# Performance work log

Hardware: AMD Instinct MI355X
Metric: run time of the kernel (lower is better)

Reference implementation:

```python
import jax, jax.numpy as jnp
import numpy as np
import math

B, S, D, H, DH = 1, 2048, 2048, 16, 64  # batch, seq, d_model, n_heads, d_head
LAMBDA_INIT = 0.8
EPS = 1e-5


def setup_inputs() -> dict:
    key = jax.random.key(0)
    ks = jax.random.split(key, 10)
    w_scale = 0.02
    inner = 2 * DH * H  # == D here
    return {
        "x": jax.random.normal(ks[0], (B, S, D), dtype=jnp.float32),
        "Wq": jax.random.normal(ks[1], (D, inner), dtype=jnp.float32) * w_scale,
        "Wk": jax.random.normal(ks[2], (D, inner), dtype=jnp.float32) * w_scale,
        "Wv": jax.random.normal(ks[3], (D, inner), dtype=jnp.float32) * w_scale,
        "Wo": jax.random.normal(ks[4], (inner, D), dtype=jnp.float32) * w_scale,
        "lambda_q1": jax.random.normal(ks[5], (DH,), dtype=jnp.float32) * 0.1,
        "lambda_k1": jax.random.normal(ks[6], (DH,), dtype=jnp.float32) * 0.1,
        "lambda_q2": jax.random.normal(ks[7], (DH,), dtype=jnp.float32) * 0.1,
        "lambda_k2": jax.random.normal(ks[8], (DH,), dtype=jnp.float32) * 0.1,
        "gn_weight": jnp.ones((inner,), dtype=jnp.float32),
        "gn_bias": jnp.zeros((inner,), dtype=jnp.float32),
    }


def reference(x, Wq, Wk, Wv, Wo, lambda_q1, lambda_k1, lambda_q2, lambda_k2,
              gn_weight, gn_bias):
    b, s, _ = x.shape
    dh = lambda_q1.shape[0]
    h = Wq.shape[1] // (2 * dh)
    scale = 1.0 / math.sqrt(dh)

    q = (x @ Wq).reshape(b, s, h, 2, dh)
    k = (x @ Wk).reshape(b, s, h, 2, dh)
    v = (x @ Wv).reshape(b, s, h, 2 * dh)

    # [B,H,S,dh]
    q1 = jnp.swapaxes(q[..., 0, :], 1, 2)
    q2 = jnp.swapaxes(q[..., 1, :], 1, 2)
    k1 = jnp.swapaxes(k[..., 0, :], 1, 2)
    k2 = jnp.swapaxes(k[..., 1, :], 1, 2)
    vh = jnp.swapaxes(v, 1, 2)  # [B,H,S,2*dh]

    score1 = jnp.einsum("bhsd,bhtd->bhst", q1, k1) * scale
    score2 = jnp.einsum("bhsd,bhtd->bhst", q2, k2) * scale
    attn1 = jax.nn.softmax(score1, axis=-1)
    attn2 = jax.nn.softmax(score2, axis=-1)

    lam = (jnp.exp(jnp.sum(lambda_q1 * lambda_k1))
           - jnp.exp(jnp.sum(lambda_q2 * lambda_k2)) + LAMBDA_INIT)

    out = jnp.einsum("bhst,bhtd->bhsd", attn1 - lam * attn2, vh)  # [B,H,S,2dh]
    out = jnp.swapaxes(out, 1, 2)  # [B,S,H,2dh]

    # GroupNorm: n_heads groups over the channel dim, per token
    mu = jnp.mean(out, axis=-1, keepdims=True)
    var = jnp.var(out, axis=-1, keepdims=True)
    out = (out - mu) * jax.lax.rsqrt(var + EPS)
    gw = gn_weight.reshape(h, 2 * dh)
    gb = gn_bias.reshape(h, 2 * dh)
    out = out * gw + gb

    out = out * (1.0 - LAMBDA_INIT)
    return out.reshape(b, s, -1) @ Wo
```

## Files before the change

kernel.cpp:

```cpp
#include <hip/hip_runtime.h>
#include <hip/hip_bf16.h>

typedef unsigned short u16;
typedef __attribute__((ext_vector_type(8))) short short8;
typedef __attribute__((ext_vector_type(4))) short short4v;
typedef __attribute__((ext_vector_type(4))) float f32x4;

#define S_DIM 2048
#define D_DIM 2048
#define H_NUM 16
#define DH_NUM 64

#if __has_builtin(__builtin_amdgcn_exp2f)
#define EXP2(x) __builtin_amdgcn_exp2f(x)
#else
#define EXP2(x) exp2f(x)
#endif

__device__ __forceinline__ u16 f2bf(float f) {
    union { float f; unsigned u; } x; x.f = f;
    unsigned r = x.u + 0x7fff + ((x.u >> 16) & 1);
    return (u16)(r >> 16);
}

__device__ __forceinline__ unsigned pk_bf16(float a, float b) {
    union { __hip_bfloat162 h; unsigned u; } cv;
    float2 t; t.x = a; t.y = b;
    cv.h = __float22bfloat162_rn(t);
    return cv.u;
}

__device__ __forceinline__ void lane_swap32(unsigned &a, unsigned &b) {
    asm("v_permlane32_swap_b32 %0, %1" : "+v"(a), "+v"(b));
}
__device__ __forceinline__ void lane_swap16(unsigned &a, unsigned &b) {
    asm("v_permlane16_swap_b32 %0, %1" : "+v"(a), "+v"(b));
}

__device__ __forceinline__ void gload16(const void* g, void* l) {
    __builtin_amdgcn_global_load_lds(
        (const __attribute__((address_space(1))) unsigned int*)g,
        (__attribute__((address_space(3))) unsigned int*)l, 16, 0, 0);
}

__device__ __forceinline__ void transpose_body(const float* __restrict__ src,
                                               u16* __restrict__ dst,
                                               int tx, int ty, int t)
{
    __shared__ float tile[64][65];
    const int r0 = ty * 64, c0 = tx * 64;
#pragma unroll
    for (int p = 0; p < 4; ++p) {
        int r = p * 16 + (t >> 4), c = (t & 15) * 4;
        float4 v = *(const float4*)&src[(long)(r0 + r) * D_DIM + c0 + c];
        tile[r][c] = v.x; tile[r][c + 1] = v.y;
        tile[r][c + 2] = v.z; tile[r][c + 3] = v.w;
    }
    __syncthreads();
#pragma unroll
    for (int p = 0; p < 2; ++p) {
        int ch = t + p * 256;
        int i = ch >> 3, j0 = (ch & 7) * 8;
        short8 o;
#pragma unroll
        for (int jj = 0; jj < 8; ++jj)
            o[jj] = (short)f2bf(tile[j0 + jj][i]);
        *(short8*)&dst[(long)(c0 + i) * D_DIM + r0 + j0] = o;
    }
}

__global__ __launch_bounds__(256)
void transpose_fast(const float* __restrict__ src, u16* __restrict__ dst)
{
    transpose_body(src, dst, blockIdx.x, blockIdx.y, threadIdx.x);
}

__global__ __launch_bounds__(256)
void prep4(const float* __restrict__ x,
           const float* __restrict__ Wq, const float* __restrict__ Wk,
           const float* __restrict__ Wv,
           u16* __restrict__ XB, u16* T0, u16* T1, u16* T2)
{
    const int z = blockIdx.z, t = threadIdx.x, bx = blockIdx.x;
    if (z == 0) {
        long i0 = ((long)bx * 256 + t) * 16;
        short8 o0, o1;
#pragma unroll
        for (int j = 0; j < 2; ++j) {
            float4 a = *(const float4*)&x[i0 + j * 8];
            float4 b = *(const float4*)&x[i0 + j * 8 + 4];
            short8& o = j ? o1 : o0;
            o[0] = (short)f2bf(a.x); o[1] = (short)f2bf(a.y);
            o[2] = (short)f2bf(a.z); o[3] = (short)f2bf(a.w);
            o[4] = (short)f2bf(b.x); o[5] = (short)f2bf(b.y);
            o[6] = (short)f2bf(b.z); o[7] = (short)f2bf(b.w);
        }
        *(short8*)&XB[i0] = o0;
        *(short8*)&XB[i0 + 8] = o1;
    } else {
        const float* src = (z == 1) ? Wq : (z == 2) ? Wk : Wv;
        u16* dst         = (z == 1) ? T0 : (z == 2) ? T1 : T2;
        transpose_body(src, dst, bx & 31, bx >> 5, t);
    }
}

__global__ __launch_bounds__(256)
void cvt_bf16(const float* __restrict__ src, u16* __restrict__ dst)
{
    int i = (blockIdx.x * 256 + threadIdx.x) * 4;
    float4 v = *(const float4*)(src + i);
    ushort4 o;
    o.x = f2bf(v.x); o.y = f2bf(v.y); o.z = f2bf(v.z); o.w = f2bf(v.w);
    *(ushort4*)(dst + i) = o;
}

__global__ __launch_bounds__(256, 2)
void gemm128(const u16* __restrict__ A,
             const u16* B0, const u16* B1, const u16* B2,
             u16* C0, u16* C1, u16* C2, int zbase)
{
    const int Kd = D_DIM, N = D_DIM, M = S_DIM;
    const int z = blockIdx.z + zbase;
    const u16* Bt = (z == 0) ? B0 : (z == 1) ? B1 : B2;
    u16* C        = (z == 0) ? C0 : (z == 1) ? C1 : C2;

    __shared__ __attribute__((aligned(16))) u16 As[128 * 64];
    __shared__ __attribute__((aligned(16))) u16 Bs[128 * 64];

    const int tid = threadIdx.x, lane = tid & 63, wave = tid >> 6;
    const int bm = blockIdx.x * 128, bn = blockIdx.y * 128;

    const int grow = lane >> 3;
    const int gcol = ((lane & 7) ^ grow) * 8;

    const int wr = (wave >> 1) * 64, wc = (wave & 1) * 64;
    const int fr = lane & 15, fq = lane >> 4;
    const int swz = fr & 7;

    f32x4 acc[4][4];
    for (int i = 0; i < 4; ++i)
        for (int j = 0; j < 4; ++j) { f32x4 zz = {0.f,0.f,0.f,0.f}; acc[i][j] = zz; }

    for (int k0 = 0; k0 < Kd; k0 += 64) {
#pragma unroll
        for (int g = 0; g < 4; ++g) {
            int r = wave * 32 + g * 8;
            gload16(A + (long)(bm + r + grow) * Kd + k0 + gcol, &As[r * 64]);
            gload16(Bt + (long)(bn + r + grow) * Kd + k0 + gcol, &Bs[r * 64]);
        }
        __syncthreads();

#pragma unroll
        for (int ks = 0; ks < 2; ++ks) {
            const int slot = ((fq + ks * 4) ^ swz) * 8;
            short8 af[4], bf[4];
#pragma unroll
            for (int i = 0; i < 4; ++i) {
                af[i] = *(const short8*)&As[(wr + i * 16 + fr) * 64 + slot];
                bf[i] = *(const short8*)&Bs[(wc + i * 16 + fr) * 64 + slot];
            }
            if (z == 2) {
#pragma unroll
                for (int i = 0; i < 4; ++i)
#pragma unroll
                    for (int j = 0; j < 4; ++j)
                        acc[i][j] = __builtin_amdgcn_mfma_f32_16x16x32_bf16(bf[j], af[i], acc[i][j], 0, 0, 0);
            } else {
#pragma unroll
                for (int i = 0; i < 4; ++i)
#pragma unroll
                    for (int j = 0; j < 4; ++j)
                        acc[i][j] = __builtin_amdgcn_mfma_f32_16x16x32_bf16(af[i], bf[j], acc[i][j], 0, 0, 0);
            }
        }
        __syncthreads();
    }

    if (z == 2) {
#pragma unroll
        for (int i = 0; i < 4; ++i) {
            int tok = bm + wr + i * 16 + fr;
#pragma unroll
            for (int j = 0; j < 4; ++j) {
                int ch = bn + wc + j * 16 + fq * 4;
#pragma unroll
                for (int r = 0; r < 4; ++r)
                    C[(long)(ch + r) * M + tok] = f2bf(acc[i][j][r]);
            }
        }
    } else {
        const float sc = (z == 0) ? 0.125f * 1.44269504f : 1.0f;
#pragma unroll
        for (int i = 0; i < 4; ++i) {
            int row = bm + wr + i * 16 + fq * 4;
#pragma unroll
            for (int j = 0; j < 4; ++j) {
                int col = bn + wc + j * 16 + fr;
#pragma unroll
                for (int r = 0; r < 4; ++r)
                    C[(long)(row + r) * N + col] = f2bf(acc[i][j][r] * sc);
            }
        }
    }
}

__global__ __launch_bounds__(256, 2)
void gemm_out(const u16* __restrict__ A, const u16* __restrict__ Bt,
              float* __restrict__ C)
{
    const int Kd = D_DIM, N = D_DIM;

    __shared__ __attribute__((aligned(16))) u16 As[64 * 64];
    __shared__ __attribute__((aligned(16))) u16 Bs[128 * 64];

    const int tid = threadIdx.x, lane = tid & 63, wave = tid >> 6;
    const int bm = blockIdx.x * 64, bn = blockIdx.y * 128;

    const int grow = lane >> 3;
    const int gcol = ((lane & 7) ^ grow) * 8;

    const int wr = (wave >> 1) * 32, wc = (wave & 1) * 64;
    const int fr = lane & 15, fq = lane >> 4;
    const int swz = fr & 7;

    f32x4 acc[2][4];
    for (int i = 0; i < 2; ++i)
        for (int j = 0; j < 4; ++j) { f32x4 zz = {0.f,0.f,0.f,0.f}; acc[i][j] = zz; }

    for (int k0 = 0; k0 < Kd; k0 += 64) {
#pragma unroll
        for (int g = 0; g < 2; ++g) {
            int r = wave * 16 + g * 8;
            gload16(A + (long)(bm + r + grow) * Kd + k0 + gcol, &As[r * 64]);
        }
#pragma unroll
        for (int g = 0; g < 4; ++g) {
            int r = wave * 32 + g * 8;
            gload16(Bt + (long)(bn + r + grow) * Kd + k0 + gcol, &Bs[r * 64]);
        }
        __syncthreads();

#pragma unroll
        for (int ks = 0; ks < 2; ++ks) {
            const int slot = ((fq + ks * 4) ^ swz) * 8;
            short8 af[2], bf[4];
#pragma unroll
            for (int i = 0; i < 2; ++i)
                af[i] = *(const short8*)&As[(wr + i * 16 + fr) * 64 + slot];
#pragma unroll
            for (int j = 0; j < 4; ++j)
                bf[j] = *(const short8*)&Bs[(wc + j * 16 + fr) * 64 + slot];
#pragma unroll
            for (int i = 0; i < 2; ++i)
#pragma unroll
                for (int j = 0; j < 4; ++j)
                    acc[i][j] = __builtin_amdgcn_mfma_f32_16x16x32_bf16(af[i], bf[j], acc[i][j], 0, 0, 0);
        }
        __syncthreads();
    }

#pragma unroll
    for (int i = 0; i < 2; ++i) {
        int row = bm + wr + i * 16 + fq * 4;
#pragma unroll
        for (int j = 0; j < 4; ++j) {
            int col = bn + wc + j * 16 + fr;
#pragma unroll
            for (int r = 0; r < 4; ++r)
                C[(long)(row + r) * N + col] = acc[i][j][r];
        }
    }
}

__global__ __launch_bounds__(256, 2)
void diff_attn(const u16* __restrict__ Qm, const u16* __restrict__ Km,
               const u16* __restrict__ Vt,
               const float* __restrict__ lq1, const float* __restrict__ lk1,
               const float* __restrict__ lq2, const float* __restrict__ lk2,
               const float* __restrict__ gw, const float* __restrict__ gb,
               u16* __restrict__ Y)
{
    __shared__ __attribute__((aligned(16))) u16 K1s[2][64 * 72];
    __shared__ __attribute__((aligned(16))) u16 K2s[2][64 * 72];
    __shared__ __attribute__((aligned(16))) u16 Vts[2][128 * 72];

    const int tid = threadIdx.x, lane = tid & 63, wave = tid >> 6;
    const int h = blockIdx.y;
    const int q0 = blockIdx.x * 64 + wave * 16;
    const int fr = lane & 15, qq = lane >> 4;

    float d1 = 0.f, d2 = 0.f;
    for (int i = 0; i < DH_NUM; ++i) {
        d1 += lq1[i] * lk1[i];
        d2 += lq2[i] * lk2[i];
    }
    const float lam = __expf(d1) - __expf(d2) + 0.8f;

    short8 q1f[2], q2f[2];
    {
        const u16* qb = Qm + (long)(q0 + fr) * D_DIM + h * 128;
        q1f[0] = *(const short8*)(qb + qq * 8);
        q1f[1] = *(const short8*)(qb + 32 + qq * 8);
        q2f[0] = *(const short8*)(qb + 64 + qq * 8);
        q2f[1] = *(const short8*)(qb + 96 + qq * 8);
    }

    f32x4 a1[8], a2[8];
    for (int n = 0; n < 8; ++n) { f32x4 zz = {0.f,0.f,0.f,0.f}; a1[n] = zz; a2[n] = zz; }
    float ls1 = 0.f, ls2 = 0.f;

    const int t0 = tid >> 3, c0 = tid & 7;
    short8 k1r[2], k2r[2], vr[4];

    auto load_tile = [&](int kb) {
        const long krow = (long)(kb * 64) * D_DIM + h * 128;
        k1r[0] = *(const short8*)&Km[krow + (long)t0 * D_DIM + c0 * 8];
        k2r[0] = *(const short8*)&Km[krow + (long)t0 * D_DIM + 64 + c0 * 8];
        k1r[1] = *(const short8*)&Km[krow + (long)(t0 + 32) * D_DIM + c0 * 8];
        k2r[1] = *(const short8*)&Km[krow + (long)(t0 + 32) * D_DIM + 64 + c0 * 8];
#pragma unroll
        for (int it = 0; it < 4; ++it)
            vr[it] = *(const short8*)&Vt[(long)(h * 128 + t0 + it * 32) * S_DIM + kb * 64 + c0 * 8];
    };
    auto store_tile = [&](int b) {
        *(short8*)&K1s[b][t0 * 72 + c0 * 8] = k1r[0];
        *(short8*)&K2s[b][t0 * 72 + c0 * 8] = k2r[0];
        *(short8*)&K1s[b][(t0 + 32) * 72 + c0 * 8] = k1r[1];
        *(short8*)&K2s[b][(t0 + 32) * 72 + c0 * 8] = k2r[1];
#pragma unroll
        for (int it = 0; it < 4; ++it)
            *(short8*)&Vts[b][(t0 + it * 32) * 72 + c0 * 8] = vr[it];
    };

    load_tile(0);
    store_tile(0);
    int p = 0;

    for (int kb = 0; kb < S_DIM / 64; ++kb) {
        __syncthreads();
        const bool more = (kb + 1 < S_DIM / 64);
        if (more) load_tile(kb + 1);

#pragma unroll
        for (int jj = 0; jj < 2; ++jj) {
            unsigned u1[2][2], u2[2][2];
#pragma unroll
            for (int jh = 0; jh < 2; ++jh) {
                const int j = jj * 2 + jh;
                f32x4 s1 = {0.f,0.f,0.f,0.f}, s2 = {0.f,0.f,0.f,0.f};
#pragma unroll
                for (int ks = 0; ks < 2; ++ks) {
                    short8 k1 = *(const short8*)&K1s[p][(j * 16 + fr) * 72 + ks * 32 + qq * 8];
                    short8 k2 = *(const short8*)&K2s[p][(j * 16 + fr) * 72 + ks * 32 + qq * 8];
                    s1 = __builtin_amdgcn_mfma_f32_16x16x32_bf16(k1, q1f[ks], s1, 0, 0, 0);
                    s2 = __builtin_amdgcn_mfma_f32_16x16x32_bf16(k2, q2f[ks], s2, 0, 0, 0);
                }
                float e1[4], e2[4];
#pragma unroll
                for (int r = 0; r < 4; ++r) {
                    e1[r] = EXP2(s1[r]);
                    e2[r] = EXP2(s2[r]);
                    ls1 += e1[r]; ls2 += e2[r];
                }
                u1[jh][0] = pk_bf16(e1[0], e1[1]); u1[jh][1] = pk_bf16(e1[2], e1[3]);
                u2[jh][0] = pk_bf16(e2[0], e2[1]); u2[jh][1] = pk_bf16(e2[2], e2[3]);
            }

            union { short8 s; unsigned u[4]; } F1, F2;
            {
                unsigned x = u1[0][0], y = u1[1][0];
                lane_swap32(x, y); lane_swap16(x, y);
                F1.u[0] = x; F1.u[2] = y;
            }
            {
                unsigned x = u1[0][1], y = u1[1][1];
                lane_swap32(x, y); lane_swap16(x, y);
                F1.u[1] = x; F1.u[3] = y;
            }
            {
                unsigned x = u2[0][0], y = u2[1][0];
                lane_swap32(x, y); lane_swap16(x, y);
                F2.u[0] = x; F2.u[2] = y;
            }
            {
                unsigned x = u2[0][1], y = u2[1][1];
                lane_swap32(x, y); lane_swap16(x, y);
                F2.u[1] = x; F2.u[3] = y;
            }

#pragma unroll
            for (int n = 0; n < 8; ++n) {
                short8 vf = *(const short8*)&Vts[p][(n * 16 + fr) * 72 + jj * 32 + qq * 8];
                a1[n] = __builtin_amdgcn_mfma_f32_16x16x32_bf16(vf, F1.s, a1[n], 0, 0, 0);
                a2[n] = __builtin_amdgcn_mfma_f32_16x16x32_bf16(vf, F2.s, a2[n], 0, 0, 0);
            }
        }

        if (more) store_tile(p ^ 1);
        p ^= 1;
    }

    float L1 = ls1, L2 = ls2;
    L1 += __shfl_xor(L1, 16, 64); L1 += __shfl_xor(L1, 32, 64);
    L2 += __shfl_xor(L2, 16, 64); L2 += __shfl_xor(L2, 32, 64);
    const float i1 = 1.f / L1, i2 = lam / L2;

    float o[8][4], sum = 0.f, sq = 0.f;
#pragma unroll
    for (int n = 0; n < 8; ++n)
#pragma unroll
        for (int r = 0; r < 4; ++r) {
            float v = a1[n][r] * i1 - a2[n][r] * i2;
            o[n][r] = v; sum += v; sq += v * v;
        }
    sum += __shfl_xor(sum, 16, 64); sum += __shfl_xor(sum, 32, 64);
    sq  += __shfl_xor(sq, 16, 64);  sq  += __shfl_xor(sq, 32, 64);
    const float mean = sum * (1.f / 128.f);
    const float var = sq * (1.f / 128.f) - mean * mean;
    const float inv = rsqrtf(var + 1e-5f);

    const long yrow = (long)(q0 + fr) * D_DIM + h * 128;
#pragma unroll
    for (int n = 0; n < 8; ++n) {
        float4 g4 = *(const float4*)&gw[h * 128 + n * 16 + qq * 4];
        float4 b4 = *(const float4*)&gb[h * 128 + n * 16 + qq * 4];
        ushort4 st;
        st.x = f2bf(((o[n][0] - mean) * inv * g4.x + b4.x) * 0.2f);
        st.y = f2bf(((o[n][1] - mean) * inv * g4.y + b4.y) * 0.2f);
        st.z = f2bf(((o[n][2] - mean) * inv * g4.z + b4.z) * 0.2f);
        st.w = f2bf(((o[n][3] - mean) * inv * g4.w + b4.w) * 0.2f);
        *(ushort4*)&Y[yrow + n * 16 + qq * 4] = st;
    }
}

extern "C" void kernel_launch(void* const* d_in, const int* in_sizes, int n_in,
                              void* d_out, int out_size, void* d_ws, size_t ws_size,
                              hipStream_t stream)
{
    const float* x   = (const float*)d_in[0];
    const float* Wq  = (const float*)d_in[1];
    const float* Wk  = (const float*)d_in[2];
    const float* Wv  = (const float*)d_in[3];
    const float* Wo  = (const float*)d_in[4];
    const float* lq1 = (const float*)d_in[5];
    const float* lk1 = (const float*)d_in[6];
    const float* lq2 = (const float*)d_in[7];
    const float* lk2 = (const float*)d_in[8];
    const float* gw  = (const float*)d_in[9];
    const float* gb  = (const float*)d_in[10];

    char* ws = (char*)d_ws;
    const size_t SEG = (size_t)D_DIM * D_DIM * sizeof(u16);
    const dim3 tgrid(32, 32), agrid(32, 16), ogrid(32, 16);

    if (ws_size >= 7 * SEG) {
        u16* XB  = (u16*)(ws + 0 * SEG);
        u16* WTq = (u16*)(ws + 1 * SEG);
        u16* WTk = (u16*)(ws + 2 * SEG);
        u16* WTv = (u16*)(ws + 3 * SEG);
        u16* Qb  = (u16*)(ws + 4 * SEG);
        u16* Kb  = (u16*)(ws + 5 * SEG);
        u16* Vt  = (u16*)(ws + 6 * SEG);
        u16* WTo = WTq;
        u16* Yb  = WTk;

        prep4<<<dim3(1024, 1, 4), 256, 0, stream>>>(x, Wq, Wk, Wv,
                                                    XB, WTq, WTk, WTv);
        gemm128<<<dim3(16, 16, 3), 256, 0, stream>>>(XB, WTq, WTk, WTv,
                                                     Qb, Kb, Vt, 0);
        transpose_fast<<<tgrid, 256, 0, stream>>>(Wo, WTo);
        diff_attn<<<agrid, 256, 0, stream>>>(Qb, Kb, Vt, lq1, lk1, lq2, lk2,
                                             gw, gb, Yb);
        gemm_out<<<ogrid, 256, 0, stream>>>(Yb, WTo, (float*)d_out);
    } else {
        u16* XB = (u16*)(ws + 0 * SEG);
        u16* WT = (u16*)(ws + 1 * SEG);
        u16* Qb = (u16*)(ws + 2 * SEG);
        u16* Kb = (u16*)(ws + 3 * SEG);
        u16* Vt = (u16*)(ws + 4 * SEG);

        cvt_bf16<<<4096, 256, 0, stream>>>(x, XB);
        transpose_fast<<<tgrid, 256, 0, stream>>>(Wq, WT);
        gemm128<<<dim3(16, 16, 1), 256, 0, stream>>>(XB, WT, WT, WT, Qb, Qb, Qb, 0);
        transpose_fast<<<tgrid, 256, 0, stream>>>(Wk, WT);
        gemm128<<<dim3(16, 16, 1), 256, 0, stream>>>(XB, WT, WT, WT, Kb, Kb, Kb, 1);
        transpose_fast<<<tgrid, 256, 0, stream>>>(Wv, WT);
        gemm128<<<dim3(16, 16, 1), 256, 0, stream>>>(XB, WT, WT, WT, Vt, Vt, Vt, 2);
        diff_attn<<<agrid, 256, 0, stream>>>(Qb, Kb, Vt, lq1, lk1, lq2, lk2,
                                             gw, gb, XB);
        transpose_fast<<<tgrid, 256, 0, stream>>>(Wo, WT);
        gemm_out<<<ogrid, 256, 0, stream>>>(XB, WT, (float*)d_out);
    }
}
```

Baseline: 303.9 us.

## Stage K/V tiles via direct global-to-LDS loads with XOR-swizzled layout

Replaces the register-staged K1/K2/Vt tile loads and the later LDS stores with direct global-to-LDS 16-byte loads (gload16) into unpadded 64-wide rows. An XOR swizzle on the 8-element column slot replaces the padding for avoiding bank conflicts. It also raises wave priority around the PV MFMA loop. The intent is to cut VGPR pressure and the LDS store instructions, and to overlap the prefetch with compute. Correctness depends on gload16's completion being covered by the single __syncthreads per iteration.

New measurement: 299.8 us. About the same (-1.3%).

```diff
diff --git a/kernel.cpp b/kernel.cpp
--- a/kernel.cpp
+++ b/kernel.cpp
@@ -280,14 +280,18 @@
                const float* __restrict__ gw, const float* __restrict__ gb,
                u16* __restrict__ Y)
 {
-    __shared__ __attribute__((aligned(16))) u16 K1s[2][64 * 72];
-    __shared__ __attribute__((aligned(16))) u16 K2s[2][64 * 72];
-    __shared__ __attribute__((aligned(16))) u16 Vts[2][128 * 72];
+    __shared__ __attribute__((aligned(16))) u16 K1s[2][64 * 64];
+    __shared__ __attribute__((aligned(16))) u16 K2s[2][64 * 64];
+    __shared__ __attribute__((aligned(16))) u16 Vts[2][128 * 64];
 
     const int tid = threadIdx.x, lane = tid & 63, wave = tid >> 6;
     const int h = blockIdx.y;
     const int q0 = blockIdx.x * 64 + wave * 16;
     const int fr = lane & 15, qq = lane >> 4;
+    const int fsw = fr & 7;
+
+    const int grow = lane >> 3;
+    const int gcol = ((lane & 7) ^ grow) * 8;
 
     float d1 = 0.f, d2 = 0.f;
     for (int i = 0; i < DH_NUM; ++i) {
@@ -309,37 +313,29 @@
     for (int n = 0; n < 8; ++n) { f32x4 zz = {0.f,0.f,0.f,0.f}; a1[n] = zz; a2[n] = zz; }
     float ls1 = 0.f, ls2 = 0.f;
 
-    const int t0 = tid >> 3, c0 = tid & 7;
-    short8 k1r[2], k2r[2], vr[4];
-
-    auto load_tile = [&](int kb) {
-        const long krow = (long)(kb * 64) * D_DIM + h * 128;
-        k1r[0] = *(const short8*)&Km[krow + (long)t0 * D_DIM + c0 * 8];
-        k2r[0] = *(const short8*)&Km[krow + (long)t0 * D_DIM + 64 + c0 * 8];
-        k1r[1] = *(const short8*)&Km[krow + (long)(t0 + 32) * D_DIM + c0 * 8];
-        k2r[1] = *(const short8*)&Km[krow + (long)(t0 + 32) * D_DIM + 64 + c0 * 8];
-#pragma unroll
-        for (int it = 0; it < 4; ++it)
-            vr[it] = *(const short8*)&Vt[(long)(h * 128 + t0 + it * 32) * S_DIM + kb * 64 + c0 * 8];
+    auto stage = [&](int kb, int b) {
+        const long kbase = (long)(kb * 64) * D_DIM + h * 128;
+#pragma unroll
+        for (int g = 0; g < 2; ++g) {
+            int r = wave * 16 + g * 8;
+            gload16(Km + kbase + (long)(r + grow) * D_DIM + gcol,      &K1s[b][r * 64]);
+            gload16(Km + kbase + (long)(r + grow) * D_DIM + 64 + gcol, &K2s[b][r * 64]);
+        }
+#pragma unroll
+        for (int g = 0; g < 4; ++g) {
+            int c = wave * 32 + g * 8;
+            gload16(Vt + (long)(h * 128 + c + grow) * S_DIM + kb * 64 + gcol,
+                    &Vts[b][c * 64]);
+        }
     };
-    auto store_tile = [&](int b) {
-        *(short8*)&K1s[b][t0 * 72 + c0 * 8] = k1r[0];
-        *(short8*)&K2s[b][t0 * 72 + c0 * 8] = k2r[0];
-        *(short8*)&K1s[b][(t0 + 32) * 72 + c0 * 8] = k1r[1];
-        *(short8*)&K2s[b][(t0 + 32) * 72 + c0 * 8] = k2r[1];
-#pragma unroll
-        for (int it = 0; it < 4; ++it)
-            *(short8*)&Vts[b][(t0 + it * 32) * 72 + c0 * 8] = vr[it];
-    };
-
-    load_tile(0);
-    store_tile(0);
+
+    stage(0, 0);
     int p = 0;
 
     for (int kb = 0; kb < S_DIM / 64; ++kb) {
         __syncthreads();
         const bool more = (kb + 1 < S_DIM / 64);
-        if (more) load_tile(kb + 1);
+        if (more) stage(kb + 1, p ^ 1);
 
 #pragma unroll
         for (int jj = 0; jj < 2; ++jj) {
@@ -350,8 +346,9 @@
                 f32x4 s1 = {0.f,0.f,0.f,0.f}, s2 = {0.f,0.f,0.f,0.f};
 #pragma unroll
                 for (int ks = 0; ks < 2; ++ks) {
-                    short8 k1 = *(const short8*)&K1s[p][(j * 16 + fr) * 72 + ks * 32 + qq * 8];
-                    short8 k2 = *(const short8*)&K2s[p][(j * 16 + fr) * 72 + ks * 32 + qq * 8];
+                    const int slot = ((ks * 4 + qq) ^ fsw) * 8;
+                    short8 k1 = *(const short8*)&K1s[p][(j * 16 + fr) * 64 + slot];
+                    short8 k2 = *(const short8*)&K2s[p][(j * 16 + fr) * 64 + slot];
                     s1 = __builtin_amdgcn_mfma_f32_16x16x32_bf16(k1, q1f[ks], s1, 0, 0, 0);
                     s2 = __builtin_amdgcn_mfma_f32_16x16x32_bf16(k2, q2f[ks], s2, 0, 0, 0);
                 }
@@ -388,15 +385,17 @@
                 F2.u[1] = x; F2.u[3] = y;
             }
 
+            const int slotV = ((jj * 4 + qq) ^ fsw) * 8;
+            __builtin_amdgcn_s_setprio(1);
 #pragma unroll
             for (int n = 0; n < 8; ++n) {
-                short8 vf = *(const short8*)&Vts[p][(n * 16 + fr) * 72 + jj * 32 + qq * 8];
+                short8 vf = *(const short8*)&Vts[p][(n * 16 + fr) * 64 + slotV];
                 a1[n] = __builtin_amdgcn_mfma_f32_16x16x32_bf16(vf, F1.s, a1[n], 0, 0, 0);
                 a2[n] = __builtin_amdgcn_mfma_f32_16x16x32_bf16(vf, F2.s, a2[n], 0, 0, 0);
             }
-        }
-
-        if (more) store_tile(p ^ 1);
+            __builtin_amdgcn_s_setprio(0);
+        }
+
         p ^= 1;
     }
 
```
